# Kernel optimization log

Measured on AMD Instinct MI355X. Metric: run time of the kernel, lower is better.

Reference implementation:

```python
import jax, jax.numpy as jnp
import numpy as np

T, B, I, H, RW, RU = 512, 64, 512, 512, 64, 64
WINIT = 0.1


def setup_inputs() -> dict:
    key = jax.random.key(0)
    ks = jax.random.split(key, 12)
    u = lambda k, shape: jax.random.uniform(k, shape, jnp.float32, -WINIT, WINIT)
    return {
        "x": jax.random.normal(ks[0], (T, B, I), jnp.float32),
        "h0": jnp.zeros((B, H), jnp.float32),
        "c0": jnp.zeros((B, H), jnp.float32),
        "U_x": u(ks[1], (I, RW)),
        "U_h": u(ks[2], (H, RU)),
        "W_x": u(ks[3], (4 * H, RW)),
        "W_h": u(ks[4], (4 * H, RU)),
        "b_x": u(ks[5], (4 * H,)),
        "b_h": u(ks[6], (4 * H,)),
        "dia_x": u(ks[7], (1, I)),
        "dia_h": u(ks[8], (1, H)),
    }


def reference(x, h0, c0, U_x, U_h, W_x, W_h, b_x, b_h, dia_x, dia_h):
    Tn, Bn, In = x.shape
    Hn = h0.shape[1]
    # Per-gate diagonal correction: sum_r U[:,r] * W[gate_slice, r] -> [4, H]
    Dx = jnp.sum(U_x[None, :, :] * W_x.reshape(4, Hn, -1), axis=-1)  # (I == H)
    Dh = jnp.sum(U_h[None, :, :] * W_h.reshape(4, Hn, -1), axis=-1)
    # Pre-batch all x-side gate pre-activations across time: [T, B, 4H]
    vm_x = jnp.tile(dia_x * x, (1, 1, 4))
    lowered_x = jnp.einsum("tbi,ir,gr->tbg", x, U_x, W_x)
    refined_x = (x[:, :, None, :] * Dx).reshape(Tn, Bn, 4 * Hn)
    gx_all = vm_x + lowered_x - refined_x + b_x

    def step(carry, gx):
        h, c = carry
        vm_h = jnp.tile(dia_h * h, (1, 4))
        lowered_h = (h @ U_h) @ W_h.T
        refined_h = (h[:, None, :] * Dh).reshape(Bn, 4 * Hn)
        g = gx + vm_h + lowered_h - refined_h + b_h
        xi, xf, xo, xn = jnp.split(g, 4, axis=1)
        i = jax.nn.sigmoid(xi)
        f = jax.nn.sigmoid(xf)
        o = jax.nn.sigmoid(xo)
        n = jnp.tanh(xn)
        c = f * c + i * n
        h = o * jnp.tanh(c)
        return (h, c), h

    (h, c), outputs = jax.lax.scan(step, (h0, c0), gx_all)
    return outputs, (h, c)
```

## Files before the change

kernel.cpp:

```cpp
#include <hip/hip_runtime.h>


typedef __fp16 h2f __attribute__((ext_vector_type(2)));
typedef unsigned int u32;
typedef unsigned short u16;

__device__ __forceinline__ float dot2f(u32 a, u32 b, float c) {
#if __has_builtin(__builtin_amdgcn_fdot2)
  return __builtin_amdgcn_fdot2(__builtin_bit_cast(h2f, a),
                                __builtin_bit_cast(h2f, b), c, false);
#else
  h2f x = __builtin_bit_cast(h2f, a);
  h2f y = __builtin_bit_cast(h2f, b);
  return c + (float)x[0] * (float)y[0] + (float)x[1] * (float)y[1];
#endif
}

__device__ __forceinline__ u32 pk2(float a, float b) {
#if __has_builtin(__builtin_amdgcn_cvt_pkrtz)
  return __builtin_bit_cast(u32, __builtin_amdgcn_cvt_pkrtz(a, b));
#else
  h2f h;
  h[0] = (__fp16)a;
  h[1] = (__fp16)b;
  return __builtin_bit_cast(u32, h);
#endif
}

__device__ __forceinline__ float h2f1(u16 u) {
  return (float)__builtin_bit_cast(__fp16, u);
}
__device__ __forceinline__ u16 f2h(float f) {
  return __builtin_bit_cast(u16, (__fp16)f);
}

__device__ __forceinline__ float dpp_xor1(float v) {
#if __has_builtin(__builtin_amdgcn_mov_dpp)
  return __builtin_bit_cast(
      float, __builtin_amdgcn_mov_dpp(__builtin_bit_cast(int, v), 0xB1, 0xF,
                                      0xF, true));
#else
  return __shfl_xor(v, 1, 64);
#endif
}

__device__ __forceinline__ void pin4(uint4& v) {
  asm volatile("" : "+v"(v.x), "+v"(v.y), "+v"(v.z), "+v"(v.w));
}

__device__ __forceinline__ void lds_barrier() {
  __builtin_amdgcn_sched_barrier(0);
  asm volatile("s_waitcnt lgkmcnt(0)" ::: "memory");
  __builtin_amdgcn_s_barrier();
  __builtin_amdgcn_sched_barrier(0);
}

__global__ void k0a_pack(const float* __restrict__ Wx, const float* __restrict__ Wh,
                         const float* __restrict__ Ux, const float* __restrict__ Uh,
                         u32* __restrict__ WxP, u32* __restrict__ WhP,
                         u32* __restrict__ UxP, u32* __restrict__ UhP) {
  int idx = blockIdx.x * 256 + threadIdx.x;
  WxP[idx] = pk2(Wx[2 * idx], Wx[2 * idx + 1]);
  WhP[idx] = pk2(Wh[2 * idx], Wh[2 * idx + 1]);
  if (idx < 16384) {
    int r = idx >> 8, k2 = idx & 255;
    UxP[idx] = pk2(Ux[(2 * k2) * 64 + r], Ux[(2 * k2 + 1) * 64 + r]);
    UhP[idx] = pk2(Uh[(2 * k2) * 64 + r], Uh[(2 * k2 + 1) * 64 + r]);
  }
}

__global__ __launch_bounds__(256) void k0b_diag(
    const float* __restrict__ Ux, const float* __restrict__ Uh,
    const float* __restrict__ Wx, const float* __restrict__ Wh,
    float* __restrict__ Dx, float* __restrict__ Dh) {
  const int t = threadIdx.x;
  const int lane = t & 63;
  const int gw = blockIdx.x * 4 + (t >> 6);
  for (int i = 0; i < 16; i++) {
    int o = gw * 16 + i;
    int which = o >> 11;
    int j = o & 2047;
    int h = j & 511;
    const float* U = which ? Uh : Ux;
    const float* W = which ? Wh : Wx;
    float v = U[h * 64 + lane] * W[j * 64 + lane];
    v += __shfl_xor(v, 1);
    v += __shfl_xor(v, 2);
    v += __shfl_xor(v, 4);
    v += __shfl_xor(v, 8);
    v += __shfl_xor(v, 16);
    v += __shfl_xor(v, 32);
    if (lane == 0) (which ? Dh : Dx)[j] = v;
  }
}

__global__ __launch_bounds__(256) void k1_xu(const float* __restrict__ x,
                                             const u32* __restrict__ UxP,
                                             u32* __restrict__ xuP) {
  __shared__ alignas(16) u32 xh[8192];
  const int tid = threadIdx.x;
  const int row0 = blockIdx.x * 32;
  const float* xs = x + (size_t)row0 * 512;

#pragma unroll
  for (int i = 0; i < 16; i++) {
    int f = tid + i * 256;
    float4 v = ((const float4*)xs)[f];
    xh[f * 2] = pk2(v.x, v.y);
    xh[f * 2 + 1] = pk2(v.z, v.w);
  }
  __syncthreads();

  const int w = tid >> 6, r = tid & 63;
  const int wr0 = w * 8;
  float acc[8] = {0.f, 0.f, 0.f, 0.f, 0.f, 0.f, 0.f, 0.f};
  const u32* Ubase = UxP + r * 256;

  for (int kc = 0; kc < 32; kc++) {
    uint4 u0 = *(const uint4*)(Ubase + kc * 8);
    uint4 u1 = *(const uint4*)(Ubase + kc * 8 + 4);
#pragma unroll
    for (int row = 0; row < 8; row++) {
      const uint4* xp = (const uint4*)&xh[(wr0 + row) * 256 + kc * 8];
      uint4 a0 = xp[0], a1 = xp[1];
      float a = acc[row];
      a = dot2f(a0.x, u0.x, a);
      a = dot2f(a0.y, u0.y, a);
      a = dot2f(a0.z, u0.z, a);
      a = dot2f(a0.w, u0.w, a);
      a = dot2f(a1.x, u1.x, a);
      a = dot2f(a1.y, u1.y, a);
      a = dot2f(a1.z, u1.z, a);
      a = dot2f(a1.w, u1.w, a);
      acc[row] = a;
    }
  }
#pragma unroll
  for (int row = 0; row < 8; row++) {
    float other = __shfl_xor(acc[row], 1, 64);
    if ((r & 1) == 0) {
      xuP[(size_t)(row0 + wr0 + row) * 32 + (r >> 1)] = pk2(acc[row], other);
    }
  }
}

__global__ __launch_bounds__(512, 2) void k2_gx(
    const float* __restrict__ x, const u32* __restrict__ xuP,
    const u32* __restrict__ WxP, const float* __restrict__ Dx,
    const float* __restrict__ bx, const float* __restrict__ diax,
    u16* __restrict__ gx) {
  __shared__ alignas(16) u32 xus[2048];
  const int t = threadIdx.x;
  const int rows0 = blockIdx.x * 64;

  uint4 Wp[4][8];
#pragma unroll
  for (int g = 0; g < 4; g++) {
    const uint4* p = (const uint4*)(WxP + (size_t)(g * 512 + t) * 32);
#pragma unroll
    for (int m = 0; m < 8; m++) Wp[g][m] = p[m];
  }
  const float dia = diax[t];
  float Dg[4], bg[4];
#pragma unroll
  for (int g = 0; g < 4; g++) {
    Dg[g] = Dx[g * 512 + t];
    bg[g] = bx[g * 512 + t];
  }
#pragma unroll
  for (int i = 0; i < 4; i++) xus[t + i * 512] = xuP[(size_t)rows0 * 32 + t + i * 512];
  __syncthreads();

  ushort4* gx4 = (ushort4*)gx;
  for (int row = 0; row < 64; row++) {
    const int R = rows0 + row;
    const uint4* s = (const uint4*)(xus + row * 32);
    float xv = x[(size_t)R * 512 + t];
    float a0 = 0.f, a1 = 0.f, a2 = 0.f, a3 = 0.f;
#pragma unroll
    for (int m = 0; m < 8; m++) {
      uint4 sm = s[m];
      uint4 w0 = Wp[0][m], w1 = Wp[1][m], w2 = Wp[2][m], w3 = Wp[3][m];
      a0 = dot2f(sm.x, w0.x, a0); a0 = dot2f(sm.y, w0.y, a0);
      a0 = dot2f(sm.z, w0.z, a0); a0 = dot2f(sm.w, w0.w, a0);
      a1 = dot2f(sm.x, w1.x, a1); a1 = dot2f(sm.y, w1.y, a1);
      a1 = dot2f(sm.z, w1.z, a1); a1 = dot2f(sm.w, w1.w, a1);
      a2 = dot2f(sm.x, w2.x, a2); a2 = dot2f(sm.y, w2.y, a2);
      a2 = dot2f(sm.z, w2.z, a2); a2 = dot2f(sm.w, w2.w, a2);
      a3 = dot2f(sm.x, w3.x, a3); a3 = dot2f(sm.y, w3.y, a3);
      a3 = dot2f(sm.z, w3.z, a3); a3 = dot2f(sm.w, w3.w, a3);
    }
    ushort4 o;
    o.x = f2h(a0 + xv * (dia - Dg[0]) + bg[0]);
    o.y = f2h(a1 + xv * (dia - Dg[1]) + bg[1]);
    o.z = f2h(a2 + xv * (dia - Dg[2]) + bg[2]);
    o.w = f2h(a3 + xv * (dia - Dg[3]) + bg[3]);
    gx4[(size_t)R * 512 + t] = o;
  }
}

__global__ __launch_bounds__(512, 2) void k3_rnn(
    const u16* __restrict__ gx, const u32* __restrict__ WhP,
    const u32* __restrict__ UhP, const float* __restrict__ Dh,
    const float* __restrict__ bh, const float* __restrict__ diah,
    float* __restrict__ out) {
  __shared__ alignas(16) u32 h32[256];
  __shared__ float partial[2][8 * 68];
  __shared__ alignas(16) u32 huW[8 * 32];

  const int t = threadIdx.x;
  const int b = blockIdx.x;
  const int lane = t & 63;
  const int w = t >> 6;

  uint4 Wp[4][8];
#pragma unroll
  for (int g = 0; g < 4; g++) {
    const uint4* p = (const uint4*)(WhP + (size_t)(g * 512 + t) * 32);
#pragma unroll
    for (int m = 0; m < 8; m++) Wp[g][m] = p[m];
  }
  uint4 Up[8];
  {
    const uint4* p = (const uint4*)(UhP + lane * 256 + w * 32);
#pragma unroll
    for (int m = 0; m < 8; m++) Up[m] = p[m];
  }
#pragma unroll
  for (int g = 0; g < 4; g++)
#pragma unroll
    for (int m = 0; m < 8; m++) pin4(Wp[g][m]);
#pragma unroll
  for (int m = 0; m < 8; m++) pin4(Up[m]);

  const float dia = diah[t];
  float Dg[4], bg[4];
#pragma unroll
  for (int g = 0; g < 4; g++) {
    Dg[g] = Dh[g * 512 + t];
    bg[g] = bh[g * 512 + t];
  }

  float h = 0.f, c = 0.f;
  if (t < 256) h32[t] = 0u;

  const ushort4* gx4 = (const ushort4*)gx;
  const size_t gbase = (size_t)b * 512 + t;
  float* outb = out + (size_t)b * 512 + t;

  ushort4 gcur = gx4[gbase];
  __syncthreads();

  for (int ts = 0; ts < 512; ts++) {
    int tn = ts + (ts < 511);
    ushort4 gnext = gx4[(size_t)tn * 32768 + gbase];
    float* part = partial[ts & 1];

    const uint4* hp = ((const uint4*)h32) + w * 8;
    float acA = 0.f, acB = 0.f;
#pragma unroll
    for (int m = 0; m < 8; m += 2) {
      uint4 h0 = hp[m], h1 = hp[m + 1];
      uint4 u0 = Up[m], u1 = Up[m + 1];
      acA = dot2f(h0.x, u0.x, acA); acB = dot2f(h1.x, u1.x, acB);
      acA = dot2f(h0.y, u0.y, acA); acB = dot2f(h1.y, u1.y, acB);
      acA = dot2f(h0.z, u0.z, acA); acB = dot2f(h1.z, u1.z, acB);
      acA = dot2f(h0.w, u0.w, acA); acB = dot2f(h1.w, u1.w, acB);
    }
    part[w * 68 + lane] = acA + acB;
    lds_barrier();

    float s0 = part[0 * 68 + lane] + part[1 * 68 + lane];
    float s1 = part[2 * 68 + lane] + part[3 * 68 + lane];
    float s2 = part[4 * 68 + lane] + part[5 * 68 + lane];
    float s3 = part[6 * 68 + lane] + part[7 * 68 + lane];
    float hu = (s0 + s1) + (s2 + s3);
    float huo = dpp_xor1(hu);
    if ((lane & 1) == 0) huW[w * 32 + (lane >> 1)] = pk2(hu, huo);
    const uint4* hup = ((const uint4*)huW) + w * 8;

    float a0 = 0.f, a1 = 0.f, a2 = 0.f, a3 = 0.f;
#pragma unroll
    for (int m = 0; m < 8; m++) {
      uint4 hm = hup[m];
      uint4 w0 = Wp[0][m], w1 = Wp[1][m], w2 = Wp[2][m], w3 = Wp[3][m];
      a0 = dot2f(hm.x, w0.x, a0); a1 = dot2f(hm.x, w1.x, a1);
      a2 = dot2f(hm.x, w2.x, a2); a3 = dot2f(hm.x, w3.x, a3);
      a0 = dot2f(hm.y, w0.y, a0); a1 = dot2f(hm.y, w1.y, a1);
      a2 = dot2f(hm.y, w2.y, a2); a3 = dot2f(hm.y, w3.y, a3);
      a0 = dot2f(hm.z, w0.z, a0); a1 = dot2f(hm.z, w1.z, a1);
      a2 = dot2f(hm.z, w2.z, a2); a3 = dot2f(hm.z, w3.z, a3);
      a0 = dot2f(hm.w, w0.w, a0); a1 = dot2f(hm.w, w1.w, a1);
      a2 = dot2f(hm.w, w2.w, a2); a3 = dot2f(hm.w, w3.w, a3);
    }
    float hd = h;
    float pre0 = a0 + h2f1(gcur.x) + hd * (dia - Dg[0]) + bg[0];
    float pre1 = a1 + h2f1(gcur.y) + hd * (dia - Dg[1]) + bg[1];
    float pre2 = a2 + h2f1(gcur.z) + hd * (dia - Dg[2]) + bg[2];
    float pre3 = a3 + h2f1(gcur.w) + hd * (dia - Dg[3]) + bg[3];

    float ig = 1.f / (1.f + __expf(-pre0));
    float fg = 1.f / (1.f + __expf(-pre1));
    float og = 1.f / (1.f + __expf(-pre2));
    float e2 = __expf(2.f * pre3);
    float ng = 1.f - 2.f / (e2 + 1.f);
    c = fg * c + ig * ng;
    float e2c = __expf(2.f * c);
    h = og * (1.f - 2.f / (e2c + 1.f));

    outb[(size_t)ts * 32768] = h;
    ((u16*)h32)[t] = f2h(h);
    gcur = gnext;
  }
  out[(size_t)512 * 32768 + (size_t)b * 512 + t] = h;
  out[(size_t)512 * 32768 + 32768 + (size_t)b * 512 + t] = c;
}

extern "C" void kernel_launch(void* const* d_in, const int* in_sizes, int n_in,
                              void* d_out, int out_size, void* d_ws,
                              size_t ws_size, hipStream_t stream) {
  const float* x = (const float*)d_in[0];
  const float* Ux = (const float*)d_in[3];
  const float* Uh = (const float*)d_in[4];
  const float* Wx = (const float*)d_in[5];
  const float* Wh = (const float*)d_in[6];
  const float* bx = (const float*)d_in[7];
  const float* bh = (const float*)d_in[8];
  const float* diax = (const float*)d_in[9];
  const float* diah = (const float*)d_in[10];
  float* out = (float*)d_out;

  char* ws = (char*)d_ws;
  u16* gx = (u16*)ws;
  u32* xuP = (u32*)(ws + 134217728);
  u32* WxP = (u32*)(ws + 138412032);
  u32* WhP = (u32*)(ws + 138674176);
  u32* UxP = (u32*)(ws + 138936320);
  u32* UhP = (u32*)(ws + 139001856);
  float* Dx = (float*)(ws + 139067392);
  float* Dh = (float*)(ws + 139075584);

  k0a_pack<<<256, 256, 0, stream>>>(Wx, Wh, Ux, Uh, WxP, WhP, UxP, UhP);
  k0b_diag<<<64, 256, 0, stream>>>(Ux, Uh, Wx, Wh, Dx, Dh);
  k1_xu<<<1024, 256, 0, stream>>>(x, UxP, xuP);
  k2_gx<<<512, 512, 0, stream>>>(x, xuP, WxP, Dx, bx, diax, gx);
  k3_rnn<<<64, 512, 0, stream>>>(gx, WhP, UhP, Dh, bh, diah, out);
}
```

Before: 897.0 us.

## Use MFMA 16x16x32 f16 for recurrent W_h projection instead of dot2 loops

Replaces the per-thread dot2 accumulation of the low-rank hidden projection (64-rank to 4x512 gates) with MFMA 16x16x32 f16 instructions. W_h fragments are laid out per wave, and the needed diagonal entries of the result tiles are scattered through a new LDS buffer so each thread can read its four gate values. This cuts the VALU instruction count on the serial recurrent step. In exchange it wastes most of each MFMA output, adds LDS traffic, and relies on wave-local ordering between the LDS writes and reads without an explicit barrier. The register pinning asm is also removed.

```diff
diff --git a/kernel.cpp b/kernel.cpp
--- a/kernel.cpp
+++ b/kernel.cpp
@@ -2,6 +2,8 @@
 
 
 typedef __fp16 h2f __attribute__((ext_vector_type(2)));
+typedef _Float16 f16x8 __attribute__((ext_vector_type(8)));
+typedef float f32x4 __attribute__((ext_vector_type(4)));
 typedef unsigned int u32;
 typedef unsigned short u16;
 
@@ -42,10 +44,6 @@
 #else
   return __shfl_xor(v, 1, 64);
 #endif
-}
-
-__device__ __forceinline__ void pin4(uint4& v) {
-  asm volatile("" : "+v"(v.x), "+v"(v.y), "+v"(v.z), "+v"(v.w));
 }
 
 __device__ __forceinline__ void lds_barrier() {
@@ -207,32 +205,32 @@
   __shared__ alignas(16) u32 h32[256];
   __shared__ float partial[2][8 * 68];
   __shared__ alignas(16) u32 huW[8 * 32];
+  __shared__ alignas(16) float preS[4 * 512];
 
   const int t = threadIdx.x;
   const int b = blockIdx.x;
   const int lane = t & 63;
   const int w = t >> 6;
-
-  uint4 Wp[4][8];
-#pragma unroll
-  for (int g = 0; g < 4; g++) {
-    const uint4* p = (const uint4*)(WhP + (size_t)(g * 512 + t) * 32);
-#pragma unroll
-    for (int m = 0; m < 8; m++) Wp[g][m] = p[m];
-  }
+  const int col = lane & 15;
+  const int rg = lane >> 4;
+
+  uint4 Wf[4][4][2];
+#pragma unroll
+  for (int g = 0; g < 4; g++)
+#pragma unroll
+    for (int jt = 0; jt < 4; jt++)
+#pragma unroll
+      for (int kh = 0; kh < 2; kh++) {
+        const u32* p = WhP +
+            ((size_t)(g * 512 + 64 * w + 16 * jt + col) * 32 + kh * 16 + rg * 4);
+        Wf[g][jt][kh] = *(const uint4*)p;
+      }
   uint4 Up[8];
   {
     const uint4* p = (const uint4*)(UhP + lane * 256 + w * 32);
 #pragma unroll
     for (int m = 0; m < 8; m++) Up[m] = p[m];
   }
-#pragma unroll
-  for (int g = 0; g < 4; g++)
-#pragma unroll
-    for (int m = 0; m < 8; m++) pin4(Wp[g][m]);
-#pragma unroll
-  for (int m = 0; m < 8; m++) pin4(Up[m]);
-
   const float dia = diah[t];
   float Dg[4], bg[4];
 #pragma unroll
@@ -277,22 +275,40 @@
     float hu = (s0 + s1) + (s2 + s3);
     float huo = dpp_xor1(hu);
     if ((lane & 1) == 0) huW[w * 32 + (lane >> 1)] = pk2(hu, huo);
-    const uint4* hup = ((const uint4*)huW) + w * 8;
-
-    float a0 = 0.f, a1 = 0.f, a2 = 0.f, a3 = 0.f;
-#pragma unroll
-    for (int m = 0; m < 8; m++) {
-      uint4 hm = hup[m];
-      uint4 w0 = Wp[0][m], w1 = Wp[1][m], w2 = Wp[2][m], w3 = Wp[3][m];
-      a0 = dot2f(hm.x, w0.x, a0); a1 = dot2f(hm.x, w1.x, a1);
-      a2 = dot2f(hm.x, w2.x, a2); a3 = dot2f(hm.x, w3.x, a3);
-      a0 = dot2f(hm.y, w0.y, a0); a1 = dot2f(hm.y, w1.y, a1);
-      a2 = dot2f(hm.y, w2.y, a2); a3 = dot2f(hm.y, w3.y, a3);
-      a0 = dot2f(hm.z, w0.z, a0); a1 = dot2f(hm.z, w1.z, a1);
-      a2 = dot2f(hm.z, w2.z, a2); a3 = dot2f(hm.z, w3.z, a3);
-      a0 = dot2f(hm.w, w0.w, a0); a1 = dot2f(hm.w, w1.w, a1);
-      a2 = dot2f(hm.w, w2.w, a2); a3 = dot2f(hm.w, w3.w, a3);
-    }
+
+    const uint4* hub = (const uint4*)(huW + w * 32);
+    f16x8 bf0 = __builtin_bit_cast(f16x8, hub[rg]);
+    f16x8 bf1 = __builtin_bit_cast(f16x8, hub[4 + rg]);
+
+#pragma unroll
+    for (int gp2 = 0; gp2 < 2; gp2++) {
+      f32x4 acc[2][4] = {};
+#pragma unroll
+      for (int g2 = 0; g2 < 2; g2++)
+#pragma unroll
+        for (int jt = 0; jt < 4; jt++) {
+          acc[g2][jt] = __builtin_amdgcn_mfma_f32_16x16x32_f16(
+              __builtin_bit_cast(f16x8, Wf[gp2 * 2 + g2][jt][0]), bf0,
+              acc[g2][jt], 0, 0, 0);
+          acc[g2][jt] = __builtin_amdgcn_mfma_f32_16x16x32_f16(
+              __builtin_bit_cast(f16x8, Wf[gp2 * 2 + g2][jt][1]), bf1,
+              acc[g2][jt], 0, 0, 0);
+        }
+#pragma unroll
+      for (int g2 = 0; g2 < 2; g2++)
+#pragma unroll
+        for (int jt = 0; jt < 4; jt++) {
+          if (col == 4 * jt + g2) {
+            ((f32x4*)preS)[(gp2 * 2 + g2) * 128 + 16 * w + 4 * jt + rg] =
+                acc[g2][jt];
+          }
+        }
+    }
+    float a0 = preS[t];
+    float a1 = preS[512 + t];
+    float a2 = preS[1024 + t];
+    float a3 = preS[1536 + t];
+
     float hd = h;
     float pre0 = a0 + h2f1(gcur.x) + hd * (dia - Dg[0]) + bg[0];
     float pre1 = a1 + h2f1(gcur.y) + hd * (dia - Dg[1]) + bg[1];
```

Result: slower. 1.113 ms (+24.1%).
